# Kernel optimization log

Hardware: AMD Instinct MI355X
Metric: run time of the kernel (lower is better)

Reference implementation:

```python
import jax, jax.numpy as jnp
import numpy as np

N, L, D = 2, 1024, 4544
H, DKV = 71, 64
ROPE_BASE = 10000.0


def _rope_tables(seq_len, head_dim, dtype):
    inv_freq = 1.0 / (ROPE_BASE ** (jnp.arange(0, head_dim, 2, dtype=jnp.float32) / head_dim))
    t = jnp.arange(seq_len, dtype=jnp.float32)
    freqs = jnp.outer(t, inv_freq)               # [L, Dkv/2]
    emb = jnp.concatenate([freqs, freqs], -1)    # [L, Dkv]
    return jnp.cos(emb).astype(dtype), jnp.sin(emb).astype(dtype)


def _apply_rotary(x, cos, sin):
    # x: [..., L, Dkv]; cos/sin: [L, Dkv] broadcast
    left, right = jnp.split(x, 2, axis=-1)
    rotated = jnp.concatenate([-right, left], axis=-1)
    return x * cos + rotated * sin


def setup_inputs() -> dict:
    key = jax.random.key(0)
    k1, k2, k3 = jax.random.split(key, 3)
    hidden_states = jax.random.normal(k1, (N, L, D), dtype=jnp.float32)
    w_qkv = jax.random.normal(k2, (D + 2 * DKV, D), dtype=jnp.float32) * (1.0 / np.sqrt(D))
    w_dense = jax.random.normal(k3, (D, D), dtype=jnp.float32) * (1.0 / np.sqrt(D))
    return {"hidden_states": hidden_states, "w_qkv": w_qkv, "w_dense": w_dense}


def reference(hidden_states, w_qkv, w_dense):
    n, l, d = hidden_states.shape
    # fused QKV projection -> [N, L, H+2, Dkv]
    fused = (hidden_states @ w_qkv.T).reshape(n, l, H + 2, DKV)
    q = fused[:, :, :-2, :]          # [N, L, H, Dkv]
    k = fused[:, :, -2, :]           # [N, L, Dkv] (single MQA kv head)
    v = fused[:, :, -1, :]           # [N, L, Dkv]

    cos, sin = _rope_tables(l, DKV, hidden_states.dtype)
    q = _apply_rotary(q, cos[:, None, :], sin[:, None, :])   # broadcast over heads
    k = _apply_rotary(k, cos, sin)

    scale = 1.0 / np.sqrt(DKV)
    # scores: [N, H, Lq, Lk]; kv head broadcast across all H query heads
    scores = jnp.einsum('nqhd,nkd->nhqk', q, k) * scale
    causal = jnp.tril(jnp.ones((l, l), dtype=bool))
    scores = jnp.where(causal, scores, jnp.finfo(scores.dtype).min)
    attn = jax.nn.softmax(scores, axis=-1)
    out = jnp.einsum('nhqk,nkd->nqhd', attn, v)              # [N, L, H, Dkv]
    out = out.reshape(n, l, H * DKV)
    return out @ w_dense.T
```

## Files before the change

kernel.cpp:

```cpp
#include <hip/hip_runtime.h>

typedef unsigned short u16;
typedef __attribute__((ext_vector_type(8))) short short8;
typedef __attribute__((ext_vector_type(4))) float floatx4;

__device__ __forceinline__ u16 f2bf(float f) {
    union { float f; unsigned int u; } v;
    v.f = f;
    unsigned int u = v.u;
    return (u16)((u + 0x7FFFu + ((u >> 16) & 1u)) >> 16);
}

__device__ __forceinline__ void cvt8_f32_bf16(const float* __restrict__ p, u16* dst) {
    const float4 x = *(const float4*)p;
    const float4 y = *(const float4*)(p + 4);
    short8 s;
    s[0] = (short)f2bf(x.x); s[1] = (short)f2bf(x.y);
    s[2] = (short)f2bf(x.z); s[3] = (short)f2bf(x.w);
    s[4] = (short)f2bf(y.x); s[5] = (short)f2bf(y.y);
    s[6] = (short)f2bf(y.z); s[7] = (short)f2bf(y.w);
    *(short8*)dst = s;
}

__device__ __forceinline__ void gld_lds16(const u16* g, u16* l) {
    __builtin_amdgcn_global_load_lds(
        (const __attribute__((address_space(1))) void*)g,
        (__attribute__((address_space(3))) void*)l,
        16, 0, 0);
}

#define DSR(dst, ptr)                                                          \
    asm volatile("ds_read_b128 %0, %1"                                         \
                 : "=v"(dst)                                                   \
                 : "v"((unsigned)(unsigned long long)(const void*)(ptr)))

__global__ __launch_bounds__(256) void cvt3_kernel(
    const float* __restrict__ a, u16* __restrict__ oa, long na,
    const float* __restrict__ b, u16* __restrict__ ob, long nb,
    const float* __restrict__ c, u16* __restrict__ oc, long nc) {
    const float* in; u16* out; long n;
    if (blockIdx.y == 0)      { in = a; out = oa; n = na; }
    else if (blockIdx.y == 1) { in = b; out = ob; n = nb; }
    else                      { in = c; out = oc; n = nc; }
    const long i = ((long)blockIdx.x * 256 + threadIdx.x) * 8;
    if (i >= n) return;
    cvt8_f32_bf16(in + i, out + i);
}


#define GEMM8P_PROLOGUE()                                                      \
    const int t    = threadIdx.x;                                              \
    const int w    = t >> 6;                                                   \
    const int lane = t & 63;                                                   \
    const int quad = lane >> 4;                                                \
    const int l16  = lane & 15;                                                \
    const int sw   = lane & 7;                                                 \
    const int qq = nwgg >> 3, rr = nwgg & 7;                                   \
    const int xcd = blockIdx.x & 7, idx = blockIdx.x >> 3;                     \
    const int wgid = (xcd < rr ? xcd * (qq + 1)                                \
                               : rr * (qq + 1) + (xcd - rr) * qq) + idx;       \
    const int m0 = (wgid / nt) * 256;                                          \
    const int n0 = (wgid % nt) * 256;                                          \
    const int wm = (w >> 2) * 128;                                             \
    const int wn = (w & 3) * 64;                                               \
    const int trow = t >> 3;                                                   \
    const int scol = ((t & 7) ^ (trow & 7)) * 8;                               \
    const long Kl = K;                                                         \
    const u16* Asrc = A + (long)(m0 + trow) * Kl + scol;                       \
    auto stageA = [&](int jt, int h, int b) {                                  \
        _Pragma("unroll")                                                      \
        for (int i = 0; i < 2; i++) {                                          \
            const u16* src = Asrc + (long)(h * 128 + i * 64) * Kl + (long)jt * 64; \
            u16* dst = &aLds[b][0] + h * 8192 + i * 4096 + t * 8;              \
            gld_lds16(src, dst);                                               \
        }                                                                      \
    };                                                                         \
    auto stageB = [&](int jt, int h, int b) {                                  \
        _Pragma("unroll")                                                      \
        for (int i = 0; i < 2; i++) {                                          \
            int rb = n0 + h * 128 + i * 64 + trow;                             \
            if (rb > N - 1) rb = N - 1;                                        \
            const u16* src = B + (long)rb * Kl + scol + (long)jt * 64;         \
            u16* dst = &bLds[b][0] + h * 8192 + i * 4096 + t * 8;              \
            gld_lds16(src, dst);                                               \
        }                                                                      \
    };                                                                         \
    floatx4 acc[8][4];                                                         \
    const floatx4 zf4 = {0.f, 0.f, 0.f, 0.f};                                  \
    _Pragma("unroll")                                                          \
    for (int i = 0; i < 8; i++)                                                \
        _Pragma("unroll")                                                      \
        for (int j = 0; j < 4; j++) acc[i][j] = zf4;                           \
                          \
    stageA(0, 0, 0); stageA(0, 1, 0);                                          \
    stageB(0, 0, 0); stageB(0, 1, 0);                                          \
    stageB(1, 0, 1); stageB(1, 1, 1);                                          \
    asm volatile("s_waitcnt vmcnt(4)" ::: "memory");                           \
    __builtin_amdgcn_s_barrier();

#define GPHASE(P, STAGE_STMT, TAIL_VM)                                         \
    {                                                                          \
        short8 afA[2], afB[2];                                                 \
        DSR(afA[0], Ac + (wm + (2 * (P)) * 16 + l16) * 64 + ((quad) ^ sw) * 8);\
        DSR(afB[0], Ac + (wm + (2 * (P) + 1) * 16 + l16) * 64 + ((quad) ^ sw) * 8); \
        DSR(afA[1], Ac + (wm + (2 * (P)) * 16 + l16) * 64 + ((4 + quad) ^ sw) * 8); \
        DSR(afB[1], Ac + (wm + (2 * (P) + 1) * 16 + l16) * 64 + ((4 + quad) ^ sw) * 8); \
        STAGE_STMT;                                                            \
        __builtin_amdgcn_s_barrier();                                          \
        asm volatile("s_waitcnt lgkmcnt(0)" ::: "memory");                     \
        __builtin_amdgcn_sched_barrier(0);                                     \
        __builtin_amdgcn_s_setprio(1);                                         \
        _Pragma("unroll")                                                      \
        for (int ks = 0; ks < 2; ks++) {                                       \
            _Pragma("unroll")                                                  \
            for (int ni = 0; ni < 4; ni++) {                                   \
                acc[2 * (P)][ni] = __builtin_amdgcn_mfma_f32_16x16x32_bf16(    \
                    afA[ks], bf[ni][ks], acc[2 * (P)][ni], 0, 0, 0);           \
                acc[2 * (P) + 1][ni] = __builtin_amdgcn_mfma_f32_16x16x32_bf16(\
                    afB[ks], bf[ni][ks], acc[2 * (P) + 1][ni], 0, 0, 0);       \
            }                                                                  \
        }                                                                      \
        __builtin_amdgcn_s_setprio(0);                                         \
        TAIL_VM;                                                               \
        __builtin_amdgcn_s_barrier();                                          \
    }

#define GEMM8P_KLOOP()                                                         \
    const int JT = K >> 6;                                                     \
    for (int j = 0; j < JT; ++j) {                                             \
        const int cur = j & 1;                                                 \
        const int nb  = cur ^ 1;                                               \
        const int jn1 = (j + 1 < JT) ? j + 1 : JT - 1;                         \
        const int jn2 = (j + 2 < JT) ? j + 2 : JT - 1;                         \
        const u16* Ac = &aLds[cur][0];                                         \
        const u16* Bc = &bLds[cur][0];                                         \
        short8 bf[4][2];                                                       \
        _Pragma("unroll")                                                      \
        for (int ni = 0; ni < 4; ni++)                                         \
            _Pragma("unroll")                                                  \
            for (int ks = 0; ks < 2; ks++)                                     \
                DSR(bf[ni][ks],                                                \
                    Bc + (wn + ni * 16 + l16) * 64 + ((4 * ks + quad) ^ sw) * 8); \
        GPHASE(0, stageA(jn1, 0, nb), );                                       \
        GPHASE(1, stageA(jn1, 1, nb), );                                       \
        GPHASE(2, stageB(jn2, 0, cur), );                                      \
        GPHASE(3, stageB(jn2, 1, cur),                                         \
               asm volatile("s_waitcnt vmcnt(4)" ::: "memory"));               \
    }                                                                          \
    asm volatile("s_waitcnt vmcnt(0)" ::: "memory");

__global__ __launch_bounds__(512, 2) void gemm_qkv_8p(
    const u16* __restrict__ A, const u16* __restrict__ B,
    u16* __restrict__ qb, u16* __restrict__ kb, u16* __restrict__ vt,
    int M, int N, int K, int nt,
    const float* __restrict__ cvt_src, u16* __restrict__ cvt_dst, long cvt_n) {
    __shared__ __align__(16) u16 aLds[2][256 * 64];
    __shared__ __align__(16) u16 bLds[2][256 * 64];
    const int nwgg = (M >> 8) * nt;
    if ((int)blockIdx.x >= nwgg) {
        const long blockbase = (long)((int)blockIdx.x - nwgg) * 16384;
#pragma unroll
        for (int u = 0; u < 4; u++) {
            const long i = blockbase + (long)u * 4096 + (long)threadIdx.x * 8;
            if (i < cvt_n) cvt8_f32_bf16(cvt_src + i, cvt_dst + i);
        }
        return;
    }
    GEMM8P_PROLOGUE()
    GEMM8P_KLOOP()

#pragma unroll
    for (int ni = 0; ni < 4; ni++) {
        const int c = n0 + wn + ni * 16 + l16;
        if (c >= N) continue;
        const int hh = c >> 6;
        const int d  = c & 63;
        float inv = 0.f;
        if (hh < 72) inv = expf((float)(2 * (d & 31)) * (-0.14391156831212787f));
#pragma unroll
        for (int mi = 0; mi < 8; mi++) {
#pragma unroll
            for (int r = 0; r < 4; r++) {
                const int row = m0 + wm + mi * 16 + quad * 4 + r;
                const int tn = row >> 10;
                const int tl = row & 1023;
                float val = acc[mi][ni][r];
                if (hh < 72) {
                    float sv, cv;
                    sincosf((float)tl * inv, &sv, &cv);
                    const float pacc = acc[mi][ni ^ 2][r];
                    val = val * cv + ((d < 32) ? -pacc : pacc) * sv;
                }
                if (hh < 71) {
                    qb[((long)((tn * 71 + hh) * 1024 + tl)) * 64 + d] = f2bf(val * 0.125f);
                } else if (hh == 71) {
                    kb[((long)(tn * 1024 + tl)) * 64 + d] = f2bf(val);
                } else {
                    vt[((long)(tn * 64 + d)) * 1024 + tl] = f2bf(val);
                }
            }
        }
    }
}

__global__ __launch_bounds__(512, 2) void gemm_dense_8p(
    const u16* __restrict__ A, const u16* __restrict__ B,
    float* __restrict__ C, int M, int N, int K, int nt) {
    __shared__ __align__(16) u16 aLds[2][256 * 64];
    __shared__ __align__(16) u16 bLds[2][256 * 64];
    const int nwgg = (M >> 8) * nt;
    GEMM8P_PROLOGUE()
    GEMM8P_KLOOP()

#pragma unroll
    for (int ni = 0; ni < 4; ni++) {
        const int col = n0 + wn + ni * 16 + l16;
        if (col >= N) continue;
#pragma unroll
        for (int mi = 0; mi < 8; mi++) {
#pragma unroll
            for (int r = 0; r < 4; r++) {
                const int row = m0 + wm + mi * 16 + quad * 4 + r;
                C[(long)row * N + col] = acc[mi][ni][r];
            }
        }
    }
}

__global__ __launch_bounds__(256) void attn_kernel2(const u16* __restrict__ qb,
                                                    const u16* __restrict__ kb,
                                                    const u16* __restrict__ vt,
                                                    u16* __restrict__ ao) {
    __shared__ __align__(16) u16 k_lds[2][64 * 72];
    __shared__ __align__(16) u16 v_lds[2][64 * 72];
    __shared__ __align__(16) u16 p_lds[4][16 * 72];
    const int qt2 = blockIdx.x;
    const int h   = blockIdx.y;
    const int n   = blockIdx.z;
    const int t    = threadIdx.x;
    const int w    = t >> 6;
    const int lane = t & 63;
    const int quad = lane >> 4;
    const int l16  = lane & 15;
    const int Q0 = qt2 * 128;

    short8 aq[2][2];
#pragma unroll
    for (int mf = 0; mf < 2; mf++) {
        const u16* qrow = qb +
            ((long)((n * 71 + h) * 1024 + Q0 + 64 * mf + w * 16 + l16)) * 64;
        aq[mf][0] = *(const short8*)(qrow + quad * 8);
        aq[mf][1] = *(const short8*)(qrow + 32 + quad * 8);
    }

    floatx4 o[2][4];
    float lst[2][4];
    const floatx4 zf4 = {0.f, 0.f, 0.f, 0.f};
#pragma unroll
    for (int mf = 0; mf < 2; mf++) {
#pragma unroll
        for (int i = 0; i < 4; i++) { o[mf][i] = zf4; lst[mf][i] = 0.f; }
    }

    const int srow = t >> 2;
    const int scol = (t & 3) * 16;
    const u16* kb_n = kb + (long)n * 1024 * 64;
    const u16* vt_n = vt + (long)n * 64 * 1024;
    u16* pw = p_lds[w];

    const int ktend = 2 * qt2 + 2;

    auto stage = [&](int kt, int b) {
        const u16* krow = kb_n + (long)(kt * 64 + srow) * 64 + scol;
        *(uint4*)(k_lds[b] + srow * 72 + scol)     = *(const uint4*)(krow);
        *(uint4*)(k_lds[b] + srow * 72 + scol + 8) = *(const uint4*)(krow + 8);
        const u16* vrow = vt_n + (long)srow * 1024 + kt * 64 + scol;
        *(uint4*)(v_lds[b] + srow * 72 + scol)     = *(const uint4*)(vrow);
        *(uint4*)(v_lds[b] + srow * 72 + scol + 8) = *(const uint4*)(vrow + 8);
    };

    stage(0, 0);
    for (int kt = 0; kt < ktend; kt++) {
        const int buf = kt & 1;
        __syncthreads();
        if (kt + 1 < ktend) stage(kt + 1, 1 - buf);

#pragma unroll
        for (int mf = 0; mf < 2; mf++) {
            if (mf == 0 && kt == 2 * qt2 + 1) continue;
            floatx4 s[4];
#pragma unroll
            for (int sub = 0; sub < 4; sub++) {
                const short8 b0 = *(const short8*)(k_lds[buf] + (sub * 16 + l16) * 72 + quad * 8);
                const short8 b1 = *(const short8*)(k_lds[buf] + (sub * 16 + l16) * 72 + 32 + quad * 8);
                floatx4 z = zf4;
                z = __builtin_amdgcn_mfma_f32_16x16x32_bf16(aq[mf][0], b0, z, 0, 0, 0);
                z = __builtin_amdgcn_mfma_f32_16x16x32_bf16(aq[mf][1], b1, z, 0, 0, 0);
                s[sub] = z;
            }
            const bool diag = (kt == 2 * qt2 + mf);
            const int rowb = Q0 + 64 * mf + w * 16 + quad * 4;
#pragma unroll
            for (int sub = 0; sub < 4; sub++) {
                const int key = kt * 64 + sub * 16 + l16;
#pragma unroll
                for (int r = 0; r < 4; r++) {
                    float p = __expf(s[sub][r]);
                    if (diag && key > rowb + r) p = 0.f;
                    lst[mf][r] += p;
                    pw[(quad * 4 + r) * 72 + sub * 16 + l16] = f2bf(p);
                }
            }
            const short8 ap0 = *(const short8*)(pw + l16 * 72 + quad * 8);
            const short8 ap1 = *(const short8*)(pw + l16 * 72 + 32 + quad * 8);
#pragma unroll
            for (int dch = 0; dch < 4; dch++) {
                const short8 bv0 = *(const short8*)(v_lds[buf] + (dch * 16 + l16) * 72 + quad * 8);
                const short8 bv1 = *(const short8*)(v_lds[buf] + (dch * 16 + l16) * 72 + 32 + quad * 8);
                o[mf][dch] = __builtin_amdgcn_mfma_f32_16x16x32_bf16(ap0, bv0, o[mf][dch], 0, 0, 0);
                o[mf][dch] = __builtin_amdgcn_mfma_f32_16x16x32_bf16(ap1, bv1, o[mf][dch], 0, 0, 0);
            }
        }
    }

    float lsum[2][4];
#pragma unroll
    for (int mf = 0; mf < 2; mf++) {
#pragma unroll
        for (int r = 0; r < 4; r++) {
            float v = lst[mf][r];
#pragma unroll
            for (int mk = 1; mk < 16; mk <<= 1) v += __shfl_xor(v, mk, 64);
            lsum[mf][r] = v;
        }
    }
#pragma unroll
    for (int mf = 0; mf < 2; mf++) {
#pragma unroll
        for (int dch = 0; dch < 4; dch++) {
#pragma unroll
            for (int r = 0; r < 4; r++) {
                const float val = o[mf][dch][r] / lsum[mf][r];
                const int row = n * 1024 + Q0 + 64 * mf + w * 16 + quad * 4 + r;
                const int col = h * 64 + dch * 16 + l16;
                ao[(long)row * 4544 + col] = f2bf(val);
            }
        }
    }
}

__global__ __launch_bounds__(256) void gemm_qkv_f32(const float* __restrict__ A,
                                                    const float* __restrict__ B,
                                                    u16* __restrict__ qb,
                                                    u16* __restrict__ kb,
                                                    u16* __restrict__ vt,
                                                    int M, int N, int K) {
    __shared__ __align__(16) u16 a_lds[128 * 32];
    __shared__ __align__(16) u16 b_lds[128 * 32];
    const int t    = threadIdx.x;
    const int lane = t & 63;
    const int w    = t >> 6;
    const int quad = lane >> 4;
    const int l16  = lane & 15;
    const int m0 = blockIdx.y * 128;
    const int n0 = blockIdx.x * 128;
    const int wm = (w >> 1) * 64;
    const int wn = (w & 1) * 64;
    const int srow = t >> 2;
    const int scol = (t & 3) * 8;
    const float* Ap0 = A + (long)(m0 + srow) * K + scol;
    const float* Ap1 = A + (long)(m0 + 64 + srow) * K + scol;
    int bn0 = n0 + srow;      if (bn0 >= N) bn0 = N - 1;
    int bn1 = n0 + 64 + srow; if (bn1 >= N) bn1 = N - 1;
    const float* Bp0 = B + (long)bn0 * K + scol;
    const float* Bp1 = B + (long)bn1 * K + scol;
    u16* as0 = a_lds + srow * 32 + scol;
    u16* as1 = a_lds + (64 + srow) * 32 + scol;
    u16* bs0 = b_lds + srow * 32 + scol;
    u16* bs1 = b_lds + (64 + srow) * 32 + scol;
    floatx4 acc[4][4];
    const floatx4 zf4 = {0.f, 0.f, 0.f, 0.f};
#pragma unroll
    for (int i = 0; i < 4; i++)
#pragma unroll
        for (int j = 0; j < 4; j++) acc[i][j] = zf4;
    for (int k0 = 0; k0 < K; k0 += 32) {
        cvt8_f32_bf16(Ap0 + k0, as0);
        cvt8_f32_bf16(Ap1 + k0, as1);
        cvt8_f32_bf16(Bp0 + k0, bs0);
        cvt8_f32_bf16(Bp1 + k0, bs1);
        __syncthreads();
        short8 af[4], bfr[4];
#pragma unroll
        for (int i = 0; i < 4; i++)
            af[i] = *(const short8*)(a_lds + (wm + i * 16 + l16) * 32 + quad * 8);
#pragma unroll
        for (int j = 0; j < 4; j++)
            bfr[j] = *(const short8*)(b_lds + (wn + j * 16 + l16) * 32 + quad * 8);
#pragma unroll
        for (int i = 0; i < 4; i++)
#pragma unroll
            for (int j = 0; j < 4; j++)
                acc[i][j] = __builtin_amdgcn_mfma_f32_16x16x32_bf16(af[i], bfr[j], acc[i][j], 0, 0, 0);
        __syncthreads();
    }
#pragma unroll
    for (int j = 0; j < 4; j++) {
        const int c = n0 + wn + j * 16 + l16;
        if (c >= N) continue;
        const int hh = c >> 6;
        const int d  = c & 63;
        float inv = 0.f;
        if (hh < 72) inv = expf((float)(2 * (d & 31)) * (-0.14391156831212787f));
#pragma unroll
        for (int i = 0; i < 4; i++) {
#pragma unroll
            for (int r = 0; r < 4; r++) {
                const int row = m0 + wm + i * 16 + quad * 4 + r;
                const int tn = row >> 10;
                const int tl = row & 1023;
                float val = acc[i][j][r];
                if (hh < 72) {
                    float sv, cv;
                    sincosf((float)tl * inv, &sv, &cv);
                    const float pacc = acc[i][j ^ 2][r];
                    val = val * cv + ((d < 32) ? -pacc : pacc) * sv;
                }
                if (hh < 71) {
                    qb[((long)((tn * 71 + hh) * 1024 + tl)) * 64 + d] = f2bf(val * 0.125f);
                } else if (hh == 71) {
                    kb[((long)(tn * 1024 + tl)) * 64 + d] = f2bf(val);
                } else {
                    vt[((long)(tn * 64 + d)) * 1024 + tl] = f2bf(val);
                }
            }
        }
    }
}

__global__ __launch_bounds__(256) void gemm_dense_f32(const u16* __restrict__ A,
                                                      const float* __restrict__ B,
                                                      float* __restrict__ C,
                                                      int M, int N, int K) {
    __shared__ __align__(16) u16 a_lds[128 * 32];
    __shared__ __align__(16) u16 b_lds[128 * 32];
    const int t    = threadIdx.x;
    const int lane = t & 63;
    const int w    = t >> 6;
    const int quad = lane >> 4;
    const int l16  = lane & 15;
    const int m0 = blockIdx.y * 128;
    const int n0 = blockIdx.x * 128;
    const int wm = (w >> 1) * 64;
    const int wn = (w & 1) * 64;
    const int srow = t >> 2;
    const int scol = (t & 3) * 8;
    const u16* Ap0 = A + (long)(m0 + srow) * K + scol;
    const u16* Ap1 = A + (long)(m0 + 64 + srow) * K + scol;
    int bn0 = n0 + srow;      if (bn0 >= N) bn0 = N - 1;
    int bn1 = n0 + 64 + srow; if (bn1 >= N) bn1 = N - 1;
    const float* Bp0 = B + (long)bn0 * K + scol;
    const float* Bp1 = B + (long)bn1 * K + scol;
    u16* as0 = a_lds + srow * 32 + scol;
    u16* as1 = a_lds + (64 + srow) * 32 + scol;
    u16* bs0 = b_lds + srow * 32 + scol;
    u16* bs1 = b_lds + (64 + srow) * 32 + scol;
    floatx4 acc[4][4];
    const floatx4 zf4 = {0.f, 0.f, 0.f, 0.f};
#pragma unroll
    for (int i = 0; i < 4; i++)
#pragma unroll
        for (int j = 0; j < 4; j++) acc[i][j] = zf4;
    for (int k0 = 0; k0 < K; k0 += 32) {
        *(uint4*)as0 = *(const uint4*)(Ap0 + k0);
        *(uint4*)as1 = *(const uint4*)(Ap1 + k0);
        cvt8_f32_bf16(Bp0 + k0, bs0);
        cvt8_f32_bf16(Bp1 + k0, bs1);
        __syncthreads();
        short8 af[4], bfr[4];
#pragma unroll
        for (int i = 0; i < 4; i++)
            af[i] = *(const short8*)(a_lds + (wm + i * 16 + l16) * 32 + quad * 8);
#pragma unroll
        for (int j = 0; j < 4; j++)
            bfr[j] = *(const short8*)(b_lds + (wn + j * 16 + l16) * 32 + quad * 8);
#pragma unroll
        for (int i = 0; i < 4; i++)
#pragma unroll
            for (int j = 0; j < 4; j++)
                acc[i][j] = __builtin_amdgcn_mfma_f32_16x16x32_bf16(af[i], bfr[j], acc[i][j], 0, 0, 0);
        __syncthreads();
    }
#pragma unroll
    for (int i = 0; i < 4; i++) {
#pragma unroll
        for (int j = 0; j < 4; j++) {
            const int col = n0 + wn + j * 16 + l16;
            if (col < N) {
#pragma unroll
                for (int r = 0; r < 4; r++) {
                    const int row = m0 + wm + i * 16 + quad * 4 + r;
                    C[(long)row * N + col] = acc[i][j][r];
                }
            }
        }
    }
}

extern "C" void kernel_launch(void* const* d_in, const int* in_sizes, int n_in,
                              void* d_out, int out_size, void* d_ws, size_t ws_size,
                              hipStream_t stream) {
    (void)in_sizes; (void)n_in; (void)out_size;
    const float* hidden  = (const float*)d_in[0];
    const float* w_qkv   = (const float*)d_in[1];
    const float* w_dense = (const float*)d_in[2];
    float* out = (float*)d_out;

    const long N_HID = (long)2048 * 4544;
    const long N_QKV = (long)4672 * 4544;
    const long N_DEN = (long)4544 * 4544;
    const long N_Q   = (long)2 * 71 * 1024 * 64;
    const long N_KV  = (long)2 * 1024 * 64;
    const long N_AO  = (long)2048 * 4544;

    const size_t needA = (size_t)(N_HID + N_QKV + N_DEN + N_Q + 2 * N_KV + N_AO) * 2;

    if (ws_size >= needA) {
        u16* hid_bf  = (u16*)d_ws;
        u16* wqkv_bf = hid_bf + N_HID;
        u16* wden_bf = wqkv_bf + N_QKV;
        u16* qbuf    = wden_bf + N_DEN;
        u16* kbuf    = qbuf + N_Q;
        u16* vtbuf   = kbuf + N_KV;
        u16* aout    = vtbuf + N_KV;

        cvt3_kernel<<<dim3(10366, 2), 256, 0, stream>>>(
            hidden, hid_bf, N_HID, w_qkv, wqkv_bf, N_QKV, w_dense, wden_bf, N_DEN);
        gemm_qkv_8p<<<dim3(8 * 19 + 1261), 512, 0, stream>>>(
            hid_bf, wqkv_bf, qbuf, kbuf, vtbuf,
            2048, 4672, 4544, 19,
            w_dense, wden_bf, N_DEN);
        attn_kernel2<<<dim3(8, 71, 2), 256, 0, stream>>>(qbuf, kbuf, vtbuf, aout);
        gemm_dense_8p<<<dim3(8 * 18), 512, 0, stream>>>(aout, wden_bf, out,
                                                        2048, 4544, 4544, 18);
    } else {
        u16* qbuf  = (u16*)d_ws;
        u16* kbuf  = qbuf + N_Q;
        u16* vtbuf = kbuf + N_KV;
        u16* aout  = vtbuf + N_KV;
        gemm_qkv_f32<<<dim3(37, 16), 256, 0, stream>>>(hidden, w_qkv,
                                                       qbuf, kbuf, vtbuf,
                                                       2048, 4672, 4544);
        attn_kernel2<<<dim3(8, 71, 2), 256, 0, stream>>>(qbuf, kbuf, vtbuf, aout);
        gemm_dense_f32<<<dim3(36, 16), 256, 0, stream>>>(aout, w_dense, out,
                                                         2048, 4544, 4544);
    }
}
```

Measured before the change: 537.2 us.

## Software-pipeline LDS A-fragment reads with MFMA phases and drop per-phase barriers

Restructures the GEMM k-loop so the LDS reads for the next A phase are issued before the MFMAs of the current phase, using partial lgkmcnt waits instead of full drains. The eight per-iteration barriers are cut to two. The aim is to hide LDS latency behind matrix math and reduce synchronisation stalls. In exchange it holds more A fragments in registers, which raises register pressure. It also relies on careful wait counts for correctness, because global loads that stage into LDS share the counters.

```diff
diff --git a/kernel.cpp b/kernel.cpp
--- a/kernel.cpp
+++ b/kernel.cpp
@@ -98,32 +98,27 @@
     asm volatile("s_waitcnt vmcnt(4)" ::: "memory");                           \
     __builtin_amdgcn_s_barrier();
 
-#define GPHASE(P, STAGE_STMT, TAIL_VM)                                         \
-    {                                                                          \
-        short8 afA[2], afB[2];                                                 \
-        DSR(afA[0], Ac + (wm + (2 * (P)) * 16 + l16) * 64 + ((quad) ^ sw) * 8);\
-        DSR(afB[0], Ac + (wm + (2 * (P) + 1) * 16 + l16) * 64 + ((quad) ^ sw) * 8); \
-        DSR(afA[1], Ac + (wm + (2 * (P)) * 16 + l16) * 64 + ((4 + quad) ^ sw) * 8); \
-        DSR(afB[1], Ac + (wm + (2 * (P) + 1) * 16 + l16) * 64 + ((4 + quad) ^ sw) * 8); \
-        STAGE_STMT;                                                            \
-        __builtin_amdgcn_s_barrier();                                          \
-        asm volatile("s_waitcnt lgkmcnt(0)" ::: "memory");                     \
-        __builtin_amdgcn_sched_barrier(0);                                     \
-        __builtin_amdgcn_s_setprio(1);                                         \
+#define ARD(P, rA, rB)                                                         \
+    DSR(rA[0], Ac + (wm + (2 * (P)) * 16 + l16) * 64 + ((quad) ^ sw) * 8);     \
+    DSR(rB[0], Ac + (wm + (2 * (P) + 1) * 16 + l16) * 64 + ((quad) ^ sw) * 8); \
+    DSR(rA[1], Ac + (wm + (2 * (P)) * 16 + l16) * 64 + ((4 + quad) ^ sw) * 8); \
+    DSR(rB[1], Ac + (wm + (2 * (P) + 1) * 16 + l16) * 64 + ((4 + quad) ^ sw) * 8);
+
+#define AMM(P, rA, rB)                                                         \
+    __builtin_amdgcn_sched_barrier(0);                                         \
+    __builtin_amdgcn_s_setprio(1);                                             \
+    _Pragma("unroll")                                                          \
+    for (int ks = 0; ks < 2; ks++) {                                           \
         _Pragma("unroll")                                                      \
-        for (int ks = 0; ks < 2; ks++) {                                       \
-            _Pragma("unroll")                                                  \
-            for (int ni = 0; ni < 4; ni++) {                                   \
-                acc[2 * (P)][ni] = __builtin_amdgcn_mfma_f32_16x16x32_bf16(    \
-                    afA[ks], bf[ni][ks], acc[2 * (P)][ni], 0, 0, 0);           \
-                acc[2 * (P) + 1][ni] = __builtin_amdgcn_mfma_f32_16x16x32_bf16(\
-                    afB[ks], bf[ni][ks], acc[2 * (P) + 1][ni], 0, 0, 0);       \
-            }                                                                  \
+        for (int ni = 0; ni < 4; ni++) {                                       \
+            acc[2 * (P)][ni] = __builtin_amdgcn_mfma_f32_16x16x32_bf16(        \
+                rA[ks], bf[ni][ks], acc[2 * (P)][ni], 0, 0, 0);                \
+            acc[2 * (P) + 1][ni] = __builtin_amdgcn_mfma_f32_16x16x32_bf16(    \
+                rB[ks], bf[ni][ks], acc[2 * (P) + 1][ni], 0, 0, 0);            \
         }                                                                      \
-        __builtin_amdgcn_s_setprio(0);                                         \
-        TAIL_VM;                                                               \
-        __builtin_amdgcn_s_barrier();                                          \
-    }
+    }                                                                          \
+    __builtin_amdgcn_s_setprio(0);                                             \
+    __builtin_amdgcn_sched_barrier(0);
 
 #define GEMM8P_KLOOP()                                                         \
     const int JT = K >> 6;                                                     \
@@ -135,17 +130,33 @@
         const u16* Ac = &aLds[cur][0];                                         \
         const u16* Bc = &bLds[cur][0];                                         \
         short8 bf[4][2];                                                       \
+        short8 aA0[2], aB0[2], aA1[2], aB1[2];                                 \
+        short8 aA2[2], aB2[2], aA3[2], aB3[2];                                 \
         _Pragma("unroll")                                                      \
         for (int ni = 0; ni < 4; ni++)                                         \
             _Pragma("unroll")                                                  \
             for (int ks = 0; ks < 2; ks++)                                     \
                 DSR(bf[ni][ks],                                                \
                     Bc + (wn + ni * 16 + l16) * 64 + ((4 * ks + quad) ^ sw) * 8); \
-        GPHASE(0, stageA(jn1, 0, nb), );                                       \
-        GPHASE(1, stageA(jn1, 1, nb), );                                       \
-        GPHASE(2, stageB(jn2, 0, cur), );                                      \
-        GPHASE(3, stageB(jn2, 1, cur),                                         \
-               asm volatile("s_waitcnt vmcnt(4)" ::: "memory"));               \
+        ARD(0, aA0, aB0)                                                       \
+        stageA(jn1, 0, nb);                                                    \
+        asm volatile("s_waitcnt lgkmcnt(0)" ::: "memory");                     \
+        ARD(1, aA1, aB1)                                                       \
+        AMM(0, aA0, aB0)                                                       \
+        stageA(jn1, 1, nb);                                                    \
+        ARD(2, aA2, aB2)                                                       \
+        asm volatile("s_waitcnt lgkmcnt(4)" ::: "memory");                     \
+        AMM(1, aA1, aB1)                                                       \
+        __builtin_amdgcn_s_barrier();    \
+        stageB(jn2, 0, cur);                                                   \
+        ARD(3, aA3, aB3)                                                       \
+        asm volatile("s_waitcnt lgkmcnt(4)" ::: "memory");                     \
+        AMM(2, aA2, aB2)                                                       \
+        stageB(jn2, 1, cur);                                                   \
+        asm volatile("s_waitcnt lgkmcnt(0)" ::: "memory");                     \
+        AMM(3, aA3, aB3)                                                       \
+        asm volatile("s_waitcnt vmcnt(4)" ::: "memory");                       \
+        __builtin_amdgcn_s_barrier();                            \
     }                                                                          \
     asm volatile("s_waitcnt vmcnt(0)" ::: "memory");
 
```

Result: no change. 527.8 us (-1.8%).
